# Kernel optimization log

Hardware: AMD Instinct MI355X
Metric: run time of the kernel (lower is better)

## Reference

```python
import jax, jax.numpy as jnp
import numpy as np

ALPHA = 0.1       # args.alpha
T = 1.0           # args.T temperature
SIGMA = 64.0      # Gaussian kernel bandwidth of kernel_function
B_CONST = 1.0     # B in get_lambda
N_ITERS = 50      # 2^-50 << tol=1e-8, matches the break condition of the 1000-iter loop
HW = 256          # image resolution (upsample target)


def _features(feat):
    # get_feature: bilinear upsample (align_corners=False == half-pixel, as jax.image.resize) then sigmoid(x/T)
    n, c, _, _ = feat.shape
    up = jax.image.resize(feat, (n, c, HW, HW), method='bilinear')
    return jax.nn.sigmoid(up / T)


def setup_inputs() -> dict:
    key = jax.random.key(0)
    k1, k2, k3, k4 = jax.random.split(key, 4)
    return {
        'cal_feat': jax.random.normal(k1, (256, 1, 64, 64), jnp.float32),
        'test_feat': jax.random.normal(k2, (32, 1, 64, 64), jnp.float32),
        'cal_gt': jax.random.randint(k3, (256, 1, 256, 256), 0, 2, jnp.int32),
        'test_gt': jax.random.randint(k4, (32, 1, 256, 256), 0, 2, jnp.int32),
    }


def reference(cal_feat, test_feat, cal_gt, test_gt):
    cal_res = _features(cal_feat)    # [N,1,H,W] in (0,1)
    test_res = _features(test_feat)  # [B,1,H,W]
    N = cal_res.shape[0]
    B = test_res.shape[0]
    f32 = cal_res.dtype

    # kernel_function.get_weight: Gaussian RBF on flattened features, plus self-weight 1, row-normalized -> [B, N+1]
    cf = cal_res.reshape(N, -1)
    tf = test_res.reshape(B, -1)
    d2 = (tf * tf).sum(-1)[:, None] + (cf * cf).sum(-1)[None, :] - 2.0 * (tf @ cf.T)
    k = jnp.exp(-d2 / (2.0 * SIGMA * SIGMA))
    w = jnp.concatenate([k, jnp.ones((B, 1), f32)], axis=1)
    w = w / w.sum(axis=1, keepdims=True)

    # FNR_i(t) = #{positive pixels of cal sample i with score < t} / #positives
    # (pred = res >= t, so false negatives are positive pixels with res < t). Precompute sorted
    # positive-pixel scores per cal sample so the bisection is a batched searchsorted.
    gt = (cal_gt > 0).reshape(N, -1)
    pos = jnp.sum(gt, axis=1)                                    # [N]
    scores = jnp.where(gt, cal_res.reshape(N, -1), jnp.inf)
    sorted_scores = jnp.sort(scores, axis=1)                     # [N, HW*HW], padding at +inf
    pos_f = jnp.maximum(pos, 1).astype(f32)

    def fnr_at(t):  # t: [B] thresholds -> [N, B]
        cnt = jax.vmap(lambda s: jnp.searchsorted(s, t, side='left'))(sorted_scores)
        return cnt.astype(f32) / pos_f[:, None]

    # batched bisection on lambda (get_lambda, vectorized over the B test samples)
    def body(carry, _):
        low, high = carry
        lam = 0.5 * (low + high)
        fnr = fnr_at(1.0 - lam)                                   # [N, B]
        risk = jnp.einsum('bn,nb->b', w[:, :-1], fnr) + w[:, -1] * B_CONST
        high = jnp.where(risk < ALPHA, lam, high)
        low = jnp.where(risk >= ALPHA, lam, low)
        return (low, high), None

    init = (jnp.zeros((B,), f32), jnp.ones((B,), f32))
    (low, _), _ = jax.lax.scan(body, init, None, length=N_ITERS)
    lam = low  # _lambda = low after the loop

    # prediction set, size and per-test FNR (get_fnr_list on the test sample)
    pred = test_res >= (1.0 - lam)[:, None, None, None]           # [B,1,H,W] bool
    size = jnp.sum(pred, axis=(1, 2, 3)).astype(f32)
    tgt = test_gt > 0
    tp = jnp.sum(pred & tgt, axis=(1, 2, 3)).astype(f32)
    tpos = jnp.maximum(jnp.sum(tgt, axis=(1, 2, 3)), 1).astype(f32)
    fnr_test = 1.0 - tp / tpos                                    # fdr_tensor, [B]
    return fnr_test, lam, size
```

## Files before the change

### kernel.cpp

```cpp
#include <hip/hip_runtime.h>


#define NPIX 65536
#define HB 16256
#define CDF_STRIDE 16272
#define ALPHA 0.1f

#define OFF_TESTRES  0
#define OFF_CALBF    8388608u
#define OFF_TESTBF   41943040u
#define OFF_GROUPED  46137344u
#define OFF_CDF      79691776u
#define OFF_GPART    96354304u
#define OFF_CC       98451456u
#define OFF_TT       98452480u
#define OFF_THR      98452608u
#define OFF_LAM      98452736u
#define OFF_FACC     98452864u

typedef __attribute__((ext_vector_type(8))) short bf16x8;
typedef __attribute__((ext_vector_type(16))) float f32x16;

__device__ __forceinline__ unsigned short f2bf_rne(float f) {
  unsigned u = __float_as_uint(f);
  return (unsigned short)((u + 0x7FFFu + ((u >> 16) & 1u)) >> 16);
}

__device__ __forceinline__ float score_at(const float* __restrict__ sfeat,
                                          int x0, int x1, float wx, int y) {
  float sy = 0.25f * (float)y - 0.375f;
  int y0 = (int)floorf(sy);
  float wy = sy - (float)y0;
  int y1 = y0 + 1;
  if (y0 < 0) y0 = 0;
  if (y1 > 63) y1 = 63;
  float a = sfeat[y0 * 64 + x0] * (1.f - wx) + sfeat[y0 * 64 + x1] * wx;
  float b = sfeat[y1 * 64 + x0] * (1.f - wx) + sfeat[y1 * 64 + x1] * wx;
  float v = a * (1.f - wy) + b * wy;
  return 1.f / (1.f + __expf(-v));
}

__global__ __launch_bounds__(1024, 8) void k_calt(const float* __restrict__ featc,
                                                  const int* __restrict__ gt,
                                                  unsigned short* __restrict__ calbf,
                                                  unsigned* __restrict__ cdf,
                                                  unsigned short* __restrict__ grouped,
                                                  float* __restrict__ cc,
                                                  const float* __restrict__ featt,
                                                  float* __restrict__ tres,
                                                  unsigned short* __restrict__ tbf,
                                                  float* __restrict__ tt) {
  __shared__ unsigned smem[16384];
  __shared__ float sfeat[4096];
  const int tid = threadIdx.x;
  const int lane = tid & 63, wv = tid >> 6;
  const int x = tid & 255, yq = tid >> 8;
  float sx = 0.25f * (float)x - 0.375f;
  int x0 = (int)floorf(sx);
  float wx = sx - (float)x0;
  int x1 = x0 + 1;
  if (x0 < 0) x0 = 0;
  if (x1 > 63) x1 = 63;

  if (blockIdx.x >= 256) {
    const int b = blockIdx.x - 256;
    for (int i = tid; i < 4096; i += 1024) sfeat[i] = featt[b * 4096 + i];
    __syncthreads();
    float* resb = tres + (size_t)b * NPIX;
    unsigned short* tbn = tbf + (size_t)b * NPIX;
    float sumsq = 0.f;
    #pragma unroll 4
    for (int it = 0; it < 64; ++it) {
      int y = it * 4 + yq;
      float s = score_at(sfeat, x0, x1, wx, y);
      int p = (y << 8) + x;
      resb[p] = s;
      unsigned short bh = f2bf_rne(s);
      tbn[p] = bh;
      float sr = __uint_as_float((unsigned)bh << 16);
      sumsq += sr * sr;
    }
    #pragma unroll
    for (int off = 32; off; off >>= 1) sumsq += __shfl_xor(sumsq, off);
    if (lane == 0) smem[wv] = __float_as_uint(sumsq);
    __syncthreads();
    if (tid == 0) {
      float t = 0.f;
      for (int w = 0; w < 16; ++w) t += __uint_as_float(smem[w]);
      tt[b] = t;
    }
    return;
  }

  const int n = blockIdx.x;
  for (int i = tid; i < HB; i += 1024) smem[i] = 0;
  for (int i = tid; i < 4096; i += 1024) sfeat[i] = featc[n * 4096 + i];
  const int* gtn = gt + (size_t)n * NPIX;
  unsigned short* cbn = calbf + (size_t)n * NPIX;
  __syncthreads();
  unsigned long long pm = 0ull;
  float sumsq = 0.f;
  #pragma unroll 4
  for (int it = 0; it < 64; ++it) {
    int y = it * 4 + yq;
    float s = score_at(sfeat, x0, x1, wx, y);
    int p = (y << 8) + x;
    unsigned short bh = f2bf_rne(s);
    cbn[p] = bh;
    float sr = __uint_as_float((unsigned)bh << 16);
    sumsq += sr * sr;
    if (gtn[p] > 0) {
      pm |= (1ull << it);
      atomicAdd(&smem[__float_as_uint(s) >> 16], 1u);
    }
  }
  #pragma unroll
  for (int off = 32; off; off >>= 1) sumsq += __shfl_xor(sumsq, off);
  if (lane == 0) smem[16336 + wv] = __float_as_uint(sumsq);
  __syncthreads();
  if (tid == 0) {
    float c = 0.f;
    for (int w = 0; w < 16; ++w) c += __uint_as_float(smem[16336 + w]);
    cc[n] = c;
  }
  unsigned* cdfn = cdf + (size_t)n * CDF_STRIDE;
  if (tid < 256) {
    const int base = tid * 64;
    unsigned psum = 0;
    if (base < HB) {
      for (int j = 0; j < 64; ++j) psum += smem[base + ((j + tid) & 63)];
    }
    unsigned inc = psum;
    #pragma unroll
    for (int off = 1; off < 64; off <<= 1) {
      unsigned v = __shfl_up(inc, off);
      if (lane >= off) inc += v;
    }
    if (lane == 63) smem[16320 + wv] = inc;
  }
  __syncthreads();
  if (tid < 256) {
    const int base = tid * 64;
    unsigned psum = 0;
    if (base < HB) {
      for (int j = 0; j < 64; ++j) psum += smem[base + ((j + tid) & 63)];
    }
    unsigned inc = psum;
    #pragma unroll
    for (int off = 1; off < 64; off <<= 1) {
      unsigned v = __shfl_up(inc, off);
      if (lane >= off) inc += v;
    }
    unsigned woff = 0;
    for (int w = 0; w < wv; ++w) woff += smem[16320 + w];
    unsigned run = woff + inc - psum;
    if (base < HB) {
      for (int j = 0; j < 64; ++j) {
        unsigned hcnt = smem[base + j];
        cdfn[base + j] = run;
        smem[base + j] = run;
        run += hcnt;
      }
    }
    if (tid == 255) cdfn[HB] = woff + inc;
  }
  __syncthreads();
  unsigned short* gn = grouped + (size_t)n * NPIX;
  for (int it = 0; it < 64; ++it) {
    if (pm & (1ull << it)) {
      int y = it * 4 + yq;
      float s = score_at(sfeat, x0, x1, wx, y);
      unsigned bits = __float_as_uint(s);
      unsigned idx = atomicAdd(&smem[bits >> 16], 1u);
      gn[idx] = (unsigned short)(bits & 0xFFFFu);
    }
  }
}

__global__ __launch_bounds__(256) void k_gemm(const unsigned short* __restrict__ tbf,
                                              const unsigned short* __restrict__ cbf,
                                              float* __restrict__ gpart) {
  __shared__ __align__(16) unsigned short As[16384];
  __shared__ __align__(16) unsigned short Bs[16384];
  __shared__ float lred[4][1024];
  const int tid = threadIdx.x;
  const int lane = tid & 63, wv = tid >> 6;
  const int r = lane & 31, half = lane >> 5;
  const int nt = blockIdx.x;
  f32x16 acc;
  #pragma unroll
  for (int i = 0; i < 16; ++i) acc[i] = 0.f;
  for (int ch = 0; ch < 2; ++ch) {
    const size_t kbase = (size_t)blockIdx.y * 1024 + ch * 512;
    __syncthreads();
    #pragma unroll
    for (int s = 0; s < 16; ++s) {
      int flat = s * 256 + tid;
      int rem = flat & 2047;
      int row = rem >> 6, kb = rem & 63;
      const unsigned short* src = (flat >= 2048)
          ? cbf + (size_t)(nt * 32 + row) * NPIX + kbase + kb * 8
          : tbf + (size_t)row * NPIX + kbase + kb * 8;
      int slot = ((kb << 5) + row) ^ (kb & 31);
      int4 v = *(const int4*)src;
      *(int4*)((flat >= 2048 ? Bs : As) + slot * 8) = v;
    }
    __syncthreads();
    #pragma unroll
    for (int i = 0; i < 8; ++i) {
      int k8 = (wv << 4) + i * 2 + half;
      int slot = ((k8 << 5) + r) ^ (k8 & 31);
      bf16x8 a = *(const bf16x8*)(As + slot * 8);
      bf16x8 b = *(const bf16x8*)(Bs + slot * 8);
      acc = __builtin_amdgcn_mfma_f32_32x32x16_bf16(a, b, acc, 0, 0, 0);
    }
  }
  #pragma unroll
  for (int rg = 0; rg < 16; ++rg) {
    int m = (rg & 3) + 8 * (rg >> 2) + 4 * half;
    lred[wv][m * 32 + r] = acc[rg];
  }
  __syncthreads();
  float* gp = gpart + (size_t)(blockIdx.y * 8 + nt) * 1024;
  for (int e = tid; e < 1024; e += 256)
    gp[e] = lred[0][e] + lred[1][e] + lred[2][e] + lred[3][e];
}

__global__ __launch_bounds__(512) void k_quant(const float* __restrict__ gpart,
                                               const float* __restrict__ cc,
                                               const float* __restrict__ tt,
                                               const unsigned* __restrict__ cdf,
                                               const unsigned short* __restrict__ grouped,
                                               float* __restrict__ lam,
                                               float* __restrict__ thr,
                                               int* __restrict__ facc) {
  __shared__ float qs[256];
  __shared__ float bins[4096];
  __shared__ float red[8];
  __shared__ float bc[2];
  __shared__ unsigned sBin;
  const int b = blockIdx.x, tid = threadIdx.x;
  const int lane = tid & 63, wv = tid >> 6;

  if (tid < 4) facc[b * 4 + tid] = 0;
  for (int i = tid; i < 4096; i += 512) bins[i] = 0.f;
  if (tid == 0) sBin = 0xFFFFFFFFu;

  float k = 0.f;
  if (tid < 256) {
    const float* gp = gpart + ((tid >> 5) * 1024) + (b * 32) + (tid & 31);
    float g = 0.f;
    #pragma unroll 8
    for (int ks = 0; ks < 64; ++ks) g += gp[(size_t)ks * 8192];
    float d2 = tt[b] + cc[tid] - 2.f * g;
    k = expf(-d2 * (1.f / 8192.f));
  }
  float v = k;
  #pragma unroll
  for (int off = 32; off; off >>= 1) v += __shfl_xor(v, off);
  if (lane == 0) red[wv] = v;
  __syncthreads();
  if (tid == 0) {
    float ws = 1.f;
    for (int w = 0; w < 8; ++w) ws += red[w];
    bc[0] = ws;
  }
  __syncthreads();
  const float wsum = bc[0];
  const float wlast = 1.f / wsum;
  const float R = ALPHA - wlast;
  if (R <= 0.f) {
    if (tid == 0) { lam[b] = 1.0f; thr[b] = 0.0f; }
    return;
  }
  if (tid < 256) {
    unsigned pos = cdf[(size_t)tid * CDF_STRIDE + HB];
    qs[tid] = k / (wsum * (float)(pos ? pos : 1u));
  }
  __syncthreads();

  int lo = 0, hi = HB;
  float baseS = 0.f;
  for (int it = 0; it < 14; ++it) {
    int mid = (lo + hi) >> 1;
    float p = 0.f;
    if (tid < 256) p = qs[tid] * (float)cdf[(size_t)tid * CDF_STRIDE + mid];
    float r = p;
    #pragma unroll
    for (int off = 32; off; off >>= 1) r += __shfl_xor(r, off);
    if (lane == 0) red[wv] = r;
    __syncthreads();
    if (tid == 0) {
      float s = 0.f;
      for (int w = 0; w < 8; ++w) s += red[w];
      bc[1] = s;
    }
    __syncthreads();
    float S = bc[1];
    if (S < R) { lo = mid; baseS = S; } else { hi = mid; }
  }
  const int B = lo;

  {
    const int n = tid >> 1;
    const float q = qs[n];
    const unsigned* cn = cdf + (size_t)n * CDF_STRIDE;
    const unsigned short* gn = grouped + (size_t)n * NPIX;
    unsigned e0 = cn[B + 1];
    for (unsigned j = cn[B] + (tid & 1); j < e0; j += 2)
      atomicAdd(&bins[gn[j] >> 4], q);
  }
  __syncthreads();

  if (wv == 0) {
    float s = 0.f;
    for (int j = 0; j < 64; ++j) s += bins[lane * 64 + j];
    float inc = s;
    #pragma unroll
    for (int off = 1; off < 64; off <<= 1) {
      float u = __shfl_up(inc, off);
      if (lane >= off) inc += u;
    }
    float pre = inc - s;
    bool hit = (baseS + pre < R) && (baseS + inc >= R);
    unsigned long long m = __ballot(hit);
    int ow = m ? (__ffsll((unsigned long long)m) - 1) : -1;
    if (lane == ow) {
      float run = baseS + pre;
      unsigned bin = (unsigned)lane * 64 + 63;
      for (int j = 0; j < 64; ++j) {
        float bv = bins[lane * 64 + j];
        if (run + bv >= R) { bin = (unsigned)lane * 64 + j; break; }
        run += bv;
      }
      sBin = bin;
    }
    if (m == 0 && lane == 0) sBin = 4095u;
  }
  __syncthreads();
  if (tid == 0) {
    unsigned tb = ((unsigned)B << 16) | (sBin << 4);
    lam[b] = 1.0f - __uint_as_float(tb | 0x8u);
    thr[b] = __uint_as_float((tb | 0xFu) + 1u);
  }
}

__global__ __launch_bounds__(256) void k_finalp(const float* __restrict__ tres,
                                                const int* __restrict__ tgt,
                                                const float* __restrict__ thr,
                                                int* __restrict__ facc) {
  __shared__ int red[12];
  const int b = blockIdx.x, seg = blockIdx.y, tid = threadIdx.x;
  const int lane = tid & 63, wv = tid >> 6;
  const float th = thr[b];
  const float* rb = tres + (size_t)b * NPIX + seg * 8192;
  const int* gb = tgt + (size_t)b * NPIX + seg * 8192;
  int sz = 0, tp = 0, tpos = 0;
  for (int i = 0; i < 32; ++i) {
    int p = i * 256 + tid;
    int pred = (rb[p] >= th) ? 1 : 0;
    int tg = (gb[p] > 0) ? 1 : 0;
    sz += pred;
    tp += pred & tg;
    tpos += tg;
  }
  #pragma unroll
  for (int off = 32; off; off >>= 1) {
    sz += __shfl_xor(sz, off);
    tp += __shfl_xor(tp, off);
    tpos += __shfl_xor(tpos, off);
  }
  if (lane == 0) { red[wv] = sz; red[4 + wv] = tp; red[8 + wv] = tpos; }
  __syncthreads();
  if (tid == 0) {
    int s0 = red[0] + red[1] + red[2] + red[3];
    int s1 = red[4] + red[5] + red[6] + red[7];
    int s2 = red[8] + red[9] + red[10] + red[11];
    atomicAdd(&facc[b * 4 + 0], s0);
    atomicAdd(&facc[b * 4 + 1], s1);
    atomicAdd(&facc[b * 4 + 2], s2);
  }
}

__global__ void k_out(const int* __restrict__ facc, const float* __restrict__ lam,
                      float* __restrict__ out) {
  int b = threadIdx.x;
  if (b < 32) {
    int sz = facc[b * 4], tp = facc[b * 4 + 1], tpos = facc[b * 4 + 2];
    float tposf = (float)(tpos > 0 ? tpos : 1);
    out[b] = 1.f - (float)tp / tposf;
    out[32 + b] = lam[b];
    out[64 + b] = (float)sz;
  }
}

extern "C" void kernel_launch(void* const* d_in, const int* in_sizes, int n_in,
                              void* d_out, int out_size, void* d_ws, size_t ws_size,
                              hipStream_t stream) {
  const float* cal_feat = (const float*)d_in[0];
  const float* test_feat = (const float*)d_in[1];
  const int* cal_gt = (const int*)d_in[2];
  const int* test_gt = (const int*)d_in[3];
  float* out = (float*)d_out;
  char* ws = (char*)d_ws;

  float* test_res = (float*)(ws + OFF_TESTRES);
  unsigned short* cal_bf = (unsigned short*)(ws + OFF_CALBF);
  unsigned short* test_bf = (unsigned short*)(ws + OFF_TESTBF);
  unsigned short* grouped = (unsigned short*)(ws + OFF_GROUPED);
  unsigned* cdf = (unsigned*)(ws + OFF_CDF);
  float* gpart = (float*)(ws + OFF_GPART);
  float* cc = (float*)(ws + OFF_CC);
  float* tt = (float*)(ws + OFF_TT);
  float* thr = (float*)(ws + OFF_THR);
  float* lam = (float*)(ws + OFF_LAM);
  int* facc = (int*)(ws + OFF_FACC);

  k_calt<<<dim3(288), dim3(1024), 0, stream>>>(cal_feat, cal_gt, cal_bf, cdf, grouped, cc,
                                               test_feat, test_res, test_bf, tt);
  k_gemm<<<dim3(8, 64), dim3(256), 0, stream>>>(test_bf, cal_bf, gpart);
  k_quant<<<dim3(32), dim3(512), 0, stream>>>(gpart, cc, tt, cdf, grouped, lam, thr, facc);
  k_finalp<<<dim3(32, 8), dim3(256), 0, stream>>>(test_res, test_gt, thr, facc);
  k_out<<<dim3(1), dim3(64), 0, stream>>>(facc, lam, out);
}
```

Baseline: 244.0 us.

## Spread test feature work across cal blocks, swizzle histogram, cache scores in registers

Removes the 32 extra test-feature blocks and has each of the 256 calibration blocks compute one eighth of a test image, so the grid is balanced. The test sum-of-squares moves into a new small kernel that reads the bf16 test features back. The LDS histogram index is XOR-swizzled to cut bank conflicts, and the second scan pass reuses stored prefixes instead of recomputing them. Scores are kept in a 64-entry register array so the scatter pass does not recompute the bilinear sigmoid, at the cost of register pressure (the launch bound is lowered from 8 to 4 minimum blocks) and one extra kernel launch.

After: 270.4 us. 1.11x slower.

```diff
diff --git a/kernel.cpp b/kernel.cpp
--- a/kernel.cpp
+++ b/kernel.cpp
@@ -25,6 +25,8 @@
   unsigned u = __float_as_uint(f);
   return (unsigned short)((u + 0x7FFFu + ((u >> 16) & 1u)) >> 16);
 }
+
+__device__ __forceinline__ int hsl(int b) { return b ^ ((b >> 6) & 31); }
 
 __device__ __forceinline__ float score_at(const float* __restrict__ sfeat,
                                           int x0, int x1, float wx, int y) {
@@ -40,7 +42,7 @@
   return 1.f / (1.f + __expf(-v));
 }
 
-__global__ __launch_bounds__(1024, 8) void k_calt(const float* __restrict__ featc,
+__global__ __launch_bounds__(1024, 4) void k_calt(const float* __restrict__ featc,
                                                   const int* __restrict__ gt,
                                                   unsigned short* __restrict__ calbf,
                                                   unsigned* __restrict__ cdf,
@@ -48,10 +50,10 @@
                                                   float* __restrict__ cc,
                                                   const float* __restrict__ featt,
                                                   float* __restrict__ tres,
-                                                  unsigned short* __restrict__ tbf,
-                                                  float* __restrict__ tt) {
-  __shared__ unsigned smem[16384];
+                                                  unsigned short* __restrict__ tbf) {
+  __shared__ unsigned smem[16704];
   __shared__ float sfeat[4096];
+  __shared__ float tfeat[4096];
   const int tid = threadIdx.x;
   const int lane = tid & 63, wv = tid >> 6;
   const int x = tid & 255, yq = tid >> 8;
@@ -62,45 +64,34 @@
   if (x0 < 0) x0 = 0;
   if (x1 > 63) x1 = 63;
 
-  if (blockIdx.x >= 256) {
-    const int b = blockIdx.x - 256;
-    for (int i = tid; i < 4096; i += 1024) sfeat[i] = featt[b * 4096 + i];
-    __syncthreads();
-    float* resb = tres + (size_t)b * NPIX;
-    unsigned short* tbn = tbf + (size_t)b * NPIX;
-    float sumsq = 0.f;
-    #pragma unroll 4
-    for (int it = 0; it < 64; ++it) {
-      int y = it * 4 + yq;
-      float s = score_at(sfeat, x0, x1, wx, y);
-      int p = (y << 8) + x;
-      resb[p] = s;
-      unsigned short bh = f2bf_rne(s);
-      tbn[p] = bh;
-      float sr = __uint_as_float((unsigned)bh << 16);
-      sumsq += sr * sr;
-    }
-    #pragma unroll
-    for (int off = 32; off; off >>= 1) sumsq += __shfl_xor(sumsq, off);
-    if (lane == 0) smem[wv] = __float_as_uint(sumsq);
-    __syncthreads();
-    if (tid == 0) {
-      float t = 0.f;
-      for (int w = 0; w < 16; ++w) t += __uint_as_float(smem[w]);
-      tt[b] = t;
-    }
-    return;
-  }
-
   const int n = blockIdx.x;
+  const int b = n >> 3, sl = n & 7;
   for (int i = tid; i < HB; i += 1024) smem[i] = 0;
-  for (int i = tid; i < 4096; i += 1024) sfeat[i] = featc[n * 4096 + i];
+  for (int i = tid; i < 4096; i += 1024) {
+    sfeat[i] = featc[n * 4096 + i];
+    tfeat[i] = featt[b * 4096 + i];
+  }
   const int* gtn = gt + (size_t)n * NPIX;
   unsigned short* cbn = calbf + (size_t)n * NPIX;
   __syncthreads();
+
+  {
+    float* resb = tres + (size_t)b * NPIX + sl * 8192;
+    unsigned short* tbn = tbf + (size_t)b * NPIX + sl * 8192;
+    #pragma unroll
+    for (int i = 0; i < 8; ++i) {
+      int y = sl * 32 + i * 4 + yq;
+      float s = score_at(tfeat, x0, x1, wx, y);
+      int q = i * 1024 + tid;
+      resb[q] = s;
+      tbn[q] = f2bf_rne(s);
+    }
+  }
+
+  unsigned sv[64];
   unsigned long long pm = 0ull;
   float sumsq = 0.f;
-  #pragma unroll 4
+  #pragma unroll
   for (int it = 0; it < 64; ++it) {
     int y = it * 4 + yq;
     float s = score_at(sfeat, x0, x1, wx, y);
@@ -109,18 +100,20 @@
     cbn[p] = bh;
     float sr = __uint_as_float((unsigned)bh << 16);
     sumsq += sr * sr;
+    unsigned bits = __float_as_uint(s);
+    sv[it] = bits;
     if (gtn[p] > 0) {
       pm |= (1ull << it);
-      atomicAdd(&smem[__float_as_uint(s) >> 16], 1u);
+      atomicAdd(&smem[hsl((int)(bits >> 16))], 1u);
     }
   }
   #pragma unroll
   for (int off = 32; off; off >>= 1) sumsq += __shfl_xor(sumsq, off);
-  if (lane == 0) smem[16336 + wv] = __float_as_uint(sumsq);
+  if (lane == 0) smem[16272 + wv] = __float_as_uint(sumsq);
   __syncthreads();
   if (tid == 0) {
     float c = 0.f;
-    for (int w = 0; w < 16; ++w) c += __uint_as_float(smem[16336 + w]);
+    for (int w = 0; w < 16; ++w) c += __uint_as_float(smem[16272 + w]);
     cc[n] = c;
   }
   unsigned* cdfn = cdf + (size_t)n * CDF_STRIDE;
@@ -128,7 +121,7 @@
     const int base = tid * 64;
     unsigned psum = 0;
     if (base < HB) {
-      for (int j = 0; j < 64; ++j) psum += smem[base + ((j + tid) & 63)];
+      for (int j = 0; j < 64; ++j) psum += smem[hsl(base + j)];
     }
     unsigned inc = psum;
     #pragma unroll
@@ -136,44 +129,62 @@
       unsigned v = __shfl_up(inc, off);
       if (lane >= off) inc += v;
     }
-    if (lane == 63) smem[16320 + wv] = inc;
+    if (lane == 63) smem[16256 + wv] = inc;
+    smem[16320 + tid] = inc - psum;
   }
   __syncthreads();
   if (tid < 256) {
+    unsigned woff = 0;
+    for (int w = 0; w < wv; ++w) woff += smem[16256 + w];
+    unsigned run = woff + smem[16320 + tid];
     const int base = tid * 64;
-    unsigned psum = 0;
-    if (base < HB) {
-      for (int j = 0; j < 64; ++j) psum += smem[base + ((j + tid) & 63)];
-    }
-    unsigned inc = psum;
-    #pragma unroll
-    for (int off = 1; off < 64; off <<= 1) {
-      unsigned v = __shfl_up(inc, off);
-      if (lane >= off) inc += v;
-    }
-    unsigned woff = 0;
-    for (int w = 0; w < wv; ++w) woff += smem[16320 + w];
-    unsigned run = woff + inc - psum;
     if (base < HB) {
       for (int j = 0; j < 64; ++j) {
-        unsigned hcnt = smem[base + j];
+        int sj = hsl(base + j);
+        unsigned hcnt = smem[sj];
         cdfn[base + j] = run;
-        smem[base + j] = run;
+        smem[sj] = run;
         run += hcnt;
       }
     }
-    if (tid == 255) cdfn[HB] = woff + inc;
+    if (tid == 0)
+      cdfn[HB] = smem[16256] + smem[16257] + smem[16258] + smem[16259];
   }
   __syncthreads();
   unsigned short* gn = grouped + (size_t)n * NPIX;
+  #pragma unroll
   for (int it = 0; it < 64; ++it) {
     if (pm & (1ull << it)) {
-      int y = it * 4 + yq;
-      float s = score_at(sfeat, x0, x1, wx, y);
-      unsigned bits = __float_as_uint(s);
-      unsigned idx = atomicAdd(&smem[bits >> 16], 1u);
+      unsigned bits = sv[it];
+      unsigned idx = atomicAdd(&smem[hsl((int)(bits >> 16))], 1u);
       gn[idx] = (unsigned short)(bits & 0xFFFFu);
     }
+  }
+}
+
+__global__ __launch_bounds__(1024) void k_tt(const unsigned short* __restrict__ tbf,
+                                             float* __restrict__ tt) {
+  __shared__ unsigned smem[16];
+  const int tid = threadIdx.x;
+  const int lane = tid & 63, wv = tid >> 6;
+  const int x = tid & 255, yq = tid >> 8;
+  const int b = blockIdx.x;
+  const unsigned short* tbn = tbf + (size_t)b * NPIX;
+  float sumsq = 0.f;
+  #pragma unroll 4
+  for (int it = 0; it < 64; ++it) {
+    int p = ((it * 4 + yq) << 8) + x;
+    float sr = __uint_as_float((unsigned)tbn[p] << 16);
+    sumsq += sr * sr;
+  }
+  #pragma unroll
+  for (int off = 32; off; off >>= 1) sumsq += __shfl_xor(sumsq, off);
+  if (lane == 0) smem[wv] = __float_as_uint(sumsq);
+  __syncthreads();
+  if (tid == 0) {
+    float t = 0.f;
+    for (int w = 0; w < 16; ++w) t += __uint_as_float(smem[w]);
+    tt[b] = t;
   }
 }
 
@@ -416,8 +427,9 @@
   float* lam = (float*)(ws + OFF_LAM);
   int* facc = (int*)(ws + OFF_FACC);
 
-  k_calt<<<dim3(288), dim3(1024), 0, stream>>>(cal_feat, cal_gt, cal_bf, cdf, grouped, cc,
-                                               test_feat, test_res, test_bf, tt);
+  k_calt<<<dim3(256), dim3(1024), 0, stream>>>(cal_feat, cal_gt, cal_bf, cdf, grouped, cc,
+                                               test_feat, test_res, test_bf);
+  k_tt<<<dim3(32), dim3(1024), 0, stream>>>(test_bf, tt);
   k_gemm<<<dim3(8, 64), dim3(256), 0, stream>>>(test_bf, cal_bf, gpart);
   k_quant<<<dim3(32), dim3(512), 0, stream>>>(gpart, cc, tt, cdf, grouped, lam, thr, facc);
   k_finalp<<<dim3(32, 8), dim3(256), 0, stream>>>(test_res, test_gt, thr, facc);
```
